# Performance work log

Hardware: AMD Instinct MI355X
Metric: run time of the kernel (lower is better)

Reference implementation:

```python
import jax, jax.numpy as jnp
import numpy as np

B, S, HID, H = 8, 1024, 1024, 16
D = HID // H  # dim per head = 64

def setup_inputs() -> dict:
    key = jax.random.key(0)
    ks = jax.random.split(key, 7)
    s = 1.0 / np.sqrt(D)  # mimic nn.Linear uniform init scale
    return {
        "sequences": jax.random.normal(ks[0], (B, S, HID), dtype=jnp.float32),
        "Wq": jax.random.uniform(ks[1], (H, D, D), jnp.float32, -s, s),
        "bq": jax.random.uniform(ks[2], (H, D), jnp.float32, -s, s),
        "Wk": jax.random.uniform(ks[3], (H, D, D), jnp.float32, -s, s),
        "bk": jax.random.uniform(ks[4], (H, D), jnp.float32, -s, s),
        "Wv": jax.random.uniform(ks[5], (H, D, D), jnp.float32, -s, s),
        "bv": jax.random.uniform(ks[6], (H, D), jnp.float32, -s, s),
    }

def reference(sequences, Wq, bq, Wk, bk, Wv, bv):
    # per-head input slice h is sequences[:, :, h*D:(h+1)*D] == reshape
    x = sequences.reshape(B, S, H, D)
    # torch Linear: y = x @ W.T + b, W is [out, in] -> einsum 'bshd,hed->bshe'
    q = jnp.einsum('bshd,hed->bshe', x, Wq) + bq
    k = jnp.einsum('bshd,hed->bshe', x, Wk) + bk
    v = jnp.einsum('bshd,hed->bshe', x, Wv) + bv
    scores = jnp.einsum('bshe,bthe->bhst', q, k) / jnp.sqrt(jnp.float32(D))
    attn = jax.nn.softmax(scores, axis=-1)  # [B,H,S,S]
    out = jnp.einsum('bhst,bthe->bshe', attn, v)
    return out.reshape(B, S, HID)  # hstack of heads == reshape
```

## Files before the change

### kernel.cpp

```cpp
#include <hip/hip_runtime.h>
#include <hip/hip_bf16.h>

#define B_   8
#define S_   1024
#define HID_ 1024
#define H_   16
#define D_   64

typedef __hip_bfloat16 bf16;
typedef __attribute__((ext_vector_type(8))) short s16x8;
typedef __attribute__((ext_vector_type(4))) float f32x4;

#define QK_BH 65536
#define V_BH  65536

__device__ __forceinline__ short f2b(float f) {
    union { float f; unsigned u; } a; a.f = f;
    return (short)((a.u + 0x8000u) >> 16);
}
__device__ __forceinline__ s16x8 cvt8(const float* p) {
    const float4* q = (const float4*)p;
    float4 u = q[0], v = q[1];
    s16x8 r;
    r[0] = f2b(u.x); r[1] = f2b(u.y); r[2] = f2b(u.z); r[3] = f2b(u.w);
    r[4] = f2b(v.x); r[5] = f2b(v.y); r[6] = f2b(v.z); r[7] = f2b(v.w);
    return r;
}
__device__ __forceinline__ s16x8 load8bf(const bf16* p) {
    return *(const s16x8*)p;
}

__device__ __forceinline__ unsigned cvtpk_bf16(float lo, float hi) {
    unsigned r;
    asm("v_cvt_pk_bf16_f32 %0, %1, %2" : "=v"(r) : "v"(lo), "v"(hi));
    return r;
}

typedef __attribute__((address_space(1))) const void gvoid_t;
typedef __attribute__((address_space(3))) void lvoid_t;
__device__ __forceinline__ void gload_lds16(const bf16* g, bf16* l) {
    __builtin_amdgcn_global_load_lds((gvoid_t*)g, (lvoid_t*)l, 16, 0, 0);
}

__global__ __launch_bounds__(256) void cvt_w(
    const float* __restrict__ Wq, const float* __restrict__ Wk,
    const float* __restrict__ Wv, bf16* __restrict__ Wf)
{
    const float* srcs[3] = {Wq, Wk, Wv};
    const float* src = srcs[blockIdx.y];
    bf16* dst = Wf + (size_t)blockIdx.y * (H_ * D_ * D_);
    const int i = blockIdx.x * 256 + threadIdx.x;
    const int h = i >> 9;
    const int r = i & 511;
    const int et = r >> 7, half = (r >> 6) & 1, lane = r & 63;
    const int quad = lane >> 4, c = lane & 15;
    const float* s = src + h * 4096 + (et * 16 + c) * 64 + half * 32 + quad * 8;
    bf16* d = dst + h * 4096 + et * 1024 + half * 512 + lane * 8;
    *(s16x8*)d = cvt8(s);
}

__global__ __launch_bounds__(256) void qkv_proj(
    const float* __restrict__ x, const bf16* __restrict__ Wf,
    const float* __restrict__ bq, const float* __restrict__ bk,
    const float* __restrict__ bv,
    bf16* __restrict__ Qf, bf16* __restrict__ Kf, bf16* __restrict__ Vf)
{
    __shared__ __align__(16) bf16 xs[64][72];

    const int id = blockIdx.x;
    const int bh_i = id & 127, sc = id >> 7;
    const int b = bh_i >> 4, h = bh_i & 15;
    const int t = threadIdx.x;
    const int wave = t >> 6, lane = t & 63;
    const int quad = lane >> 4, c = lane & 15;
    const size_t bh = (size_t)bh_i;

    {
        const float* xg = x + ((size_t)b * S_ + sc * 64) * HID_ + h * D_;
#pragma unroll
        for (int i = 0; i < 4; ++i) {
            const int j = i * 256 + t;
            const int row = j >> 4, seg = j & 15;
            float4 v = *(const float4*)(xg + (size_t)row * HID_ + seg * 4);
            short4 pk;
            pk.x = f2b(v.x); pk.y = f2b(v.y); pk.z = f2b(v.z); pk.w = f2b(v.w);
            *(short4*)&xs[row][seg * 4] = pk;
        }
    }
    __syncthreads();

    s16x8 xa0 = *(const s16x8*)&xs[wave * 16 + c][quad * 8];
    s16x8 xa1 = *(const s16x8*)&xs[wave * 16 + c][32 + quad * 8];

    const float* bs[3] = {bq, bk, bv};

#pragma unroll
    for (int m = 0; m < 3; ++m) {
        const bf16*  Wm   = Wf + ((size_t)m * H_ + h) * 4096;
        const float* bias = bs[m] + h * D_;
#pragma unroll
        for (int et = 0; et < 4; ++et) {
            s16x8 wf0 = load8bf(Wm + et * 1024 + lane * 8);
            s16x8 wf1 = load8bf(Wm + et * 1024 + 512 + lane * 8);
            if (m < 2) {
                const int hp = et >> 1;
                const int qp = (2 * et + (quad >> 1)) & 3;
                const float4 bb = *(const float4*)&bias[et * 16 + quad * 4];
                f32x4 acc = {0.f, 0.f, 0.f, 0.f};
                acc = __builtin_amdgcn_mfma_f32_16x16x32_bf16(wf0, xa0, acc, 0, 0, 0);
                acc = __builtin_amdgcn_mfma_f32_16x16x32_bf16(wf1, xa1, acc, 0, 0, 0);
                const int ts = sc * 4 + wave;
                bf16* dst = (m == 0 ? Qf : Kf) + bh * QK_BH + ts * 1024 +
                            hp * 512 + (qp * 16 + c) * 8 + (quad & 1) * 4;
                short4 pk;
                pk.x = f2b(acc[0] + bb.x);
                pk.y = f2b(acc[1] + bb.y);
                pk.z = f2b(acc[2] + bb.z);
                pk.w = f2b(acc[3] + bb.w);
                *(short4*)dst = pk;
            } else {
                const float bbv = bias[et * 16 + c];
                f32x4 acc = {0.f, 0.f, 0.f, 0.f};
                acc = __builtin_amdgcn_mfma_f32_16x16x32_bf16(xa0, wf0, acc, 0, 0, 0);
                acc = __builtin_amdgcn_mfma_f32_16x16x32_bf16(xa1, wf1, acc, 0, 0, 0);
                bf16* dst = Vf + bh * V_BH + sc * 4096 + et * 1024 +
                            (wave >> 1) * 512 + (quad * 16 + c) * 8 + (wave & 1) * 4;
                short4 pk;
                pk.x = f2b(acc[0] + bbv);
                pk.y = f2b(acc[1] + bbv);
                pk.z = f2b(acc[2] + bbv);
                pk.w = f2b(acc[3] + bbv);
                *(short4*)dst = pk;
            }
        }
    }
}

__global__ __launch_bounds__(256, 2) void attn(
    const bf16* __restrict__ Qf, const bf16* __restrict__ Kf,
    const bf16* __restrict__ Vf, float* __restrict__ out)
{
    __shared__ __align__(16) union {
        bf16  kv[2][8192];
        float os[4][16][68];
    } sm;

    const int id = blockIdx.x;
    const int bh_i = id & 127, qc = id >> 7;
    const int b = bh_i >> 4, h = bh_i & 15;
    const int wave = threadIdx.x >> 6, lane = threadIdx.x & 63;
    const int quad = lane >> 4, c = lane & 15;
    const int ts0 = qc * 16 + wave * 4;
    const size_t bh = (size_t)bh_i;

    s16x8 aq[4][2];
#pragma unroll
    for (int mt = 0; mt < 4; ++mt) {
        const bf16* Qb = Qf + bh * QK_BH + (ts0 + mt) * 1024 + lane * 8;
        aq[mt][0] = load8bf(Qb);
        aq[mt][1] = load8bf(Qb + 512);
    }

    const f32x4 zero4 = {0.f, 0.f, 0.f, 0.f};
    f32x4 o[4][4];
    f32x4 ld4[4];
#pragma unroll
    for (int mt = 0; mt < 4; ++mt) {
        ld4[mt] = zero4;
#pragma unroll
        for (int et = 0; et < 4; ++et) o[mt][et] = zero4;
    }

    s16x8 ones;
#pragma unroll
    for (int j = 0; j < 8; ++j) ones[j] = (short)0x3F80;

    const float CEXP = 0.18033688011112042f;
    const float NM0  = -16.0f * 0.18033688011112042f;

    const bf16* Kg = Kf + bh * QK_BH;
    const bf16* Vg = Vf + bh * V_BH;

    auto STAGE = [&](int kt, int bi) {
#pragma unroll
        for (int i = 0; i < 4; ++i) {
            const int ch = wave * 4 + i;
            const bf16* src = (ch < 8
                ? Kg + (size_t)kt * 4096 + ch * 512
                : Vg + (size_t)kt * 4096 + (ch - 8) * 512) + lane * 8;
            gload_lds16(src, &sm.kv[bi][ch * 512]);
        }
    };

    STAGE(0, 0);
    __syncthreads();

    int cur = 0;
#pragma unroll 1
    for (int kt = 0; kt < S_ / 64; ++kt) {
        if (kt < S_ / 64 - 1) STAGE(kt + 1, cur ^ 1);

        const bf16* kb = &sm.kv[cur][0];
        const bf16* vb = &sm.kv[cur][4096];

        s16x8 ka[4], kb2[4];
#pragma unroll
        for (int ct = 0; ct < 4; ++ct) {
            ka[ct]  = load8bf(kb + ct * 1024 + lane * 8);
            kb2[ct] = load8bf(kb + ct * 1024 + 512 + lane * 8);
        }
        s16x8 vf4[4][2];
#pragma unroll
        for (int et = 0; et < 4; ++et)
#pragma unroll
            for (int p = 0; p < 2; ++p)
                vf4[et][p] = load8bf(vb + et * 1024 + p * 512 + lane * 8);

#pragma unroll
        for (int mt = 0; mt < 4; ++mt) {
            f32x4 s4[4];
#pragma unroll
            for (int ct = 0; ct < 4; ++ct) {
                f32x4 acc = zero4;
                acc = __builtin_amdgcn_mfma_f32_16x16x32_bf16(ka[ct],  aq[mt][0], acc, 0, 0, 0);
                acc = __builtin_amdgcn_mfma_f32_16x16x32_bf16(kb2[ct], aq[mt][1], acc, 0, 0, 0);
                s4[ct] = acc;
            }
            s16x8 pz[2];
#pragma unroll
            for (int p = 0; p < 2; ++p) {
                float pa[4], pb[4];
#pragma unroll
                for (int j = 0; j < 4; ++j) {
                    pa[j] = __builtin_amdgcn_exp2f(fmaf(s4[2 * p][j],     CEXP, NM0));
                    pb[j] = __builtin_amdgcn_exp2f(fmaf(s4[2 * p + 1][j], CEXP, NM0));
                }
                union { unsigned u[4]; s16x8 v; } z;
                z.u[0] = cvtpk_bf16(pa[0], pa[1]);
                z.u[1] = cvtpk_bf16(pa[2], pa[3]);
                z.u[2] = cvtpk_bf16(pb[0], pb[1]);
                z.u[3] = cvtpk_bf16(pb[2], pb[3]);
                pz[p] = z.v;
            }
            ld4[mt] = __builtin_amdgcn_mfma_f32_16x16x32_bf16(pz[0], ones, ld4[mt], 0, 0, 0);
            ld4[mt] = __builtin_amdgcn_mfma_f32_16x16x32_bf16(pz[1], ones, ld4[mt], 0, 0, 0);
#pragma unroll
            for (int et = 0; et < 4; ++et) {
                o[mt][et] = __builtin_amdgcn_mfma_f32_16x16x32_bf16(pz[0], vf4[et][0], o[mt][et], 0, 0, 0);
                o[mt][et] = __builtin_amdgcn_mfma_f32_16x16x32_bf16(pz[1], vf4[et][1], o[mt][et], 0, 0, 0);
            }
        }
        __syncthreads();
        cur ^= 1;
    }

#pragma unroll
    for (int mt = 0; mt < 4; ++mt) {
        float inv[4];
#pragma unroll
        for (int r = 0; r < 4; ++r) inv[r] = 1.0f / ld4[mt][r];
#pragma unroll
        for (int et = 0; et < 4; ++et)
#pragma unroll
            for (int r = 0; r < 4; ++r)
                sm.os[wave][quad * 4 + r][et * 16 + c] = o[mt][et][r] * inv[r];
        float* orow = out + ((size_t)b * S_ + (ts0 + mt) * 16 + c) * HID_ + h * D_;
#pragma unroll
        for (int j = 0; j < 4; ++j) {
            float4 v = *(const float4*)&sm.os[wave][c][(quad + j * 4) * 4];
            *(float4*)(orow + (quad + j * 4) * 4) = v;
        }
    }
}

extern "C" void kernel_launch(void* const* d_in, const int* in_sizes, int n_in,
                              void* d_out, int out_size, void* d_ws, size_t ws_size,
                              hipStream_t stream) {
    (void)in_sizes; (void)n_in; (void)out_size; (void)ws_size;
    const float* x  = (const float*)d_in[0];
    const float* Wq = (const float*)d_in[1];
    const float* bq = (const float*)d_in[2];
    const float* Wk = (const float*)d_in[3];
    const float* bk = (const float*)d_in[4];
    const float* Wv = (const float*)d_in[5];
    const float* bv = (const float*)d_in[6];
    float* outp = (float*)d_out;

    bf16* Qfw = (bf16*)d_ws;
    bf16* Kfw = Qfw + (size_t)128 * QK_BH;
    bf16* Vfw = Kfw + (size_t)128 * QK_BH;
    bf16* Wfw = Vfw + (size_t)128 * V_BH;

    cvt_w<<<dim3(32, 3), 256, 0, stream>>>(Wq, Wk, Wv, Wfw);
    qkv_proj<<<dim3(2048), 256, 0, stream>>>(x, Wfw, bq, bk, bv, Qfw, Kfw, Vfw);
    attn<<<dim3(512), 256, 0, stream>>>(Qfw, Kfw, Vfw, outp);
}
```

Baseline: 146.2 us.

## Load K/V fragments directly from global memory and halve query tile per block

Drops the LDS double-buffered global_load_lds staging of K/V tiles and the per-iteration block barrier, so each wave reads its MFMA fragments straight from global memory (through L2/L1). Each wave now handles 2 query tiles instead of 4, and the grid doubles to 1024 blocks, which raises parallelism and lowers register pressure. The cost is that every wave fetches K/V independently, so cache traffic per block goes up and K/V reuse across query tiles is halved.

Result: slower. 156.7 us (+7.2%).

```diff
diff --git a/kernel.cpp b/kernel.cpp
--- a/kernel.cpp
+++ b/kernel.cpp
@@ -34,12 +34,6 @@
     unsigned r;
     asm("v_cvt_pk_bf16_f32 %0, %1, %2" : "=v"(r) : "v"(lo), "v"(hi));
     return r;
-}
-
-typedef __attribute__((address_space(1))) const void gvoid_t;
-typedef __attribute__((address_space(3))) void lvoid_t;
-__device__ __forceinline__ void gload_lds16(const bf16* g, bf16* l) {
-    __builtin_amdgcn_global_load_lds((gvoid_t*)g, (lvoid_t*)l, 16, 0, 0);
 }
 
 __global__ __launch_bounds__(256) void cvt_w(
@@ -140,32 +134,29 @@
     const bf16* __restrict__ Qf, const bf16* __restrict__ Kf,
     const bf16* __restrict__ Vf, float* __restrict__ out)
 {
-    __shared__ __align__(16) union {
-        bf16  kv[2][8192];
-        float os[4][16][68];
-    } sm;
+    __shared__ __align__(16) float os[4][16][68];
 
     const int id = blockIdx.x;
     const int bh_i = id & 127, qc = id >> 7;
     const int b = bh_i >> 4, h = bh_i & 15;
     const int wave = threadIdx.x >> 6, lane = threadIdx.x & 63;
     const int quad = lane >> 4, c = lane & 15;
-    const int ts0 = qc * 16 + wave * 4;
+    const int ts0 = qc * 8 + wave * 2;
     const size_t bh = (size_t)bh_i;
 
-    s16x8 aq[4][2];
-#pragma unroll
-    for (int mt = 0; mt < 4; ++mt) {
+    s16x8 aq[2][2];
+#pragma unroll
+    for (int mt = 0; mt < 2; ++mt) {
         const bf16* Qb = Qf + bh * QK_BH + (ts0 + mt) * 1024 + lane * 8;
         aq[mt][0] = load8bf(Qb);
         aq[mt][1] = load8bf(Qb + 512);
     }
 
     const f32x4 zero4 = {0.f, 0.f, 0.f, 0.f};
-    f32x4 o[4][4];
-    f32x4 ld4[4];
-#pragma unroll
-    for (int mt = 0; mt < 4; ++mt) {
+    f32x4 o[2][4];
+    f32x4 ld4[2];
+#pragma unroll
+    for (int mt = 0; mt < 2; ++mt) {
         ld4[mt] = zero4;
 #pragma unroll
         for (int et = 0; et < 4; ++et) o[mt][et] = zero4;
@@ -178,46 +169,26 @@
     const float CEXP = 0.18033688011112042f;
     const float NM0  = -16.0f * 0.18033688011112042f;
 
-    const bf16* Kg = Kf + bh * QK_BH;
-    const bf16* Vg = Vf + bh * V_BH;
-
-    auto STAGE = [&](int kt, int bi) {
-#pragma unroll
-        for (int i = 0; i < 4; ++i) {
-            const int ch = wave * 4 + i;
-            const bf16* src = (ch < 8
-                ? Kg + (size_t)kt * 4096 + ch * 512
-                : Vg + (size_t)kt * 4096 + (ch - 8) * 512) + lane * 8;
-            gload_lds16(src, &sm.kv[bi][ch * 512]);
-        }
-    };
-
-    STAGE(0, 0);
-    __syncthreads();
-
-    int cur = 0;
+    const bf16* Kb = Kf + bh * QK_BH + lane * 8;
+    const bf16* Vb = Vf + bh * V_BH  + lane * 8;
+
 #pragma unroll 1
     for (int kt = 0; kt < S_ / 64; ++kt) {
-        if (kt < S_ / 64 - 1) STAGE(kt + 1, cur ^ 1);
-
-        const bf16* kb = &sm.kv[cur][0];
-        const bf16* vb = &sm.kv[cur][4096];
-
         s16x8 ka[4], kb2[4];
 #pragma unroll
         for (int ct = 0; ct < 4; ++ct) {
-            ka[ct]  = load8bf(kb + ct * 1024 + lane * 8);
-            kb2[ct] = load8bf(kb + ct * 1024 + 512 + lane * 8);
+            ka[ct]  = load8bf(Kb + (kt * 4 + ct) * 1024);
+            kb2[ct] = load8bf(Kb + (kt * 4 + ct) * 1024 + 512);
         }
         s16x8 vf4[4][2];
 #pragma unroll
         for (int et = 0; et < 4; ++et)
 #pragma unroll
             for (int p = 0; p < 2; ++p)
-                vf4[et][p] = load8bf(vb + et * 1024 + p * 512 + lane * 8);
-
-#pragma unroll
-        for (int mt = 0; mt < 4; ++mt) {
+                vf4[et][p] = load8bf(Vb + kt * 4096 + et * 1024 + p * 512);
+
+#pragma unroll
+        for (int mt = 0; mt < 2; ++mt) {
             f32x4 s4[4];
 #pragma unroll
             for (int ct = 0; ct < 4; ++ct) {
@@ -250,12 +221,10 @@
                 o[mt][et] = __builtin_amdgcn_mfma_f32_16x16x32_bf16(pz[1], vf4[et][1], o[mt][et], 0, 0, 0);
             }
         }
-        __syncthreads();
-        cur ^= 1;
-    }
-
-#pragma unroll
-    for (int mt = 0; mt < 4; ++mt) {
+    }
+
+#pragma unroll
+    for (int mt = 0; mt < 2; ++mt) {
         float inv[4];
 #pragma unroll
         for (int r = 0; r < 4; ++r) inv[r] = 1.0f / ld4[mt][r];
@@ -263,11 +232,11 @@
         for (int et = 0; et < 4; ++et)
 #pragma unroll
             for (int r = 0; r < 4; ++r)
-                sm.os[wave][quad * 4 + r][et * 16 + c] = o[mt][et][r] * inv[r];
+                os[wave][quad * 4 + r][et * 16 + c] = o[mt][et][r] * inv[r];
         float* orow = out + ((size_t)b * S_ + (ts0 + mt) * 16 + c) * HID_ + h * D_;
 #pragma unroll
         for (int j = 0; j < 4; ++j) {
-            float4 v = *(const float4*)&sm.os[wave][c][(quad + j * 4) * 4];
+            float4 v = *(const float4*)&os[wave][c][(quad + j * 4) * 4];
             *(float4*)(orow + (quad + j * 4) * 4) = v;
         }
     }
@@ -293,5 +262,5 @@
 
     cvt_w<<<dim3(32, 3), 256, 0, stream>>>(Wq, Wk, Wv, Wfw);
     qkv_proj<<<dim3(2048), 256, 0, stream>>>(x, Wfw, bq, bk, bv, Qfw, Kfw, Vfw);
-    attn<<<dim3(512), 256, 0, stream>>>(Qfw, Kfw, Vfw, outp);
-}
+    attn<<<dim3(1024), 256, 0, stream>>>(Qfw, Kfw, Vfw, outp);
+}
```
